# Performance work log

Measured on AMD Instinct MI355X. Metric: run time of the kernel, lower is better.

## Reference

```python
import jax, jax.numpy as jnp
import numpy as np

B, L, D, H = 2, 2048, 1024, 16
HD = D // H
HID = 4 * D
EPS = 1e-5


def setup_inputs() -> dict:
    key = jax.random.key(0)
    ks = jax.random.split(key, 16)
    s = 0.02
    inp = {
        "x": jax.random.normal(ks[0], (B, L, D), jnp.float32),
        "mask": jnp.triu(jnp.ones((L, L), bool), k=1),  # True above diagonal -> masked
        "wq": jax.random.normal(ks[1], (D, D), jnp.float32) * s,
        "wk": jax.random.normal(ks[2], (D, D), jnp.float32) * s,
        "wv": jax.random.normal(ks[3], (D, D), jnp.float32) * s,
        "wo": jax.random.normal(ks[4], (D, D), jnp.float32) * s,
        "ln1_g": jnp.ones((D,), jnp.float32),
        "ln1_b": jnp.zeros((D,), jnp.float32),
        "ln2_g": jnp.ones((D,), jnp.float32),
        "ln2_b": jnp.zeros((D,), jnp.float32),
        "w1": jax.random.normal(ks[5], (HID, D), jnp.float32) * s,
        "b1": jnp.zeros((HID,), jnp.float32),
        "wg": jax.random.normal(ks[6], (HID, D), jnp.float32) * s,
        "w2": jax.random.normal(ks[7], (D, HID), jnp.float32) * s,
        "b2": jnp.zeros((D,), jnp.float32),
    }
    return inp


def _layernorm(x, g, b):
    mu = jnp.mean(x, axis=-1, keepdims=True)
    var = jnp.mean(jnp.square(x - mu), axis=-1, keepdims=True)
    return (x - mu) * jax.lax.rsqrt(var + EPS) * g + b


def _attention(h, mask, wq, wk, wv, wo):
    b, l, d = h.shape
    scale = HD ** -0.5
    # torch Linear: y = x @ W.T (W is [out, in])
    q = (h @ wq.T).reshape(b, l, H, HD)
    k = (h @ wk.T).reshape(b, l, H, HD)
    v = (h @ wv.T).reshape(b, l, H, HD)
    attn = jnp.einsum("bqhd,bkhd->bhqk", q, k) * scale
    attn = jnp.where(mask[None, None, :, :], -jnp.inf, attn)
    pos_bias = jnp.arange(l, dtype=attn.dtype) * 0.01  # additive bias along key axis
    attn = attn + pos_bias[None, None, None, :]
    attn = jax.nn.softmax(attn, axis=-1)
    out = jnp.einsum("bhqk,bkhd->bqhd", attn, v).reshape(b, l, d)
    return out @ wo.T


def _ffn(h, w1, b1, wg, w2, b2):
    return (jax.nn.silu(h @ w1.T + b1) * (h @ wg.T)) @ w2.T + b2


def reference(x, mask, wq, wk, wv, wo, ln1_g, ln1_b, ln2_g, ln2_b, w1, b1, wg, w2, b2):
    x = x + _attention(_layernorm(x, ln1_g, ln1_b), mask, wq, wk, wv, wo)
    x = x + _ffn(_layernorm(x, ln2_g, ln2_b), w1, b1, wg, w2, b2)
    return x
```

## Files before the change

### kernel.cpp

```cpp
#include <hip/hip_runtime.h>

#define ML   2048
#define MD   1024
#define MH   16
#define MHD  64
#define MB   2
#define MM   4096
#define MHID 4096

typedef unsigned short u16;
typedef short bf16x8 __attribute__((ext_vector_type(8)));
typedef float f32x4 __attribute__((ext_vector_type(4)));

__device__ __forceinline__ u16 f2bf(float f) {
    union { float f; unsigned u; } c; c.f = f;
    unsigned r = c.u + 0x7fffu + ((c.u >> 16) & 1u);
    return (u16)(r >> 16);
}
__device__ __forceinline__ float bf2f(u16 h) {
    union { unsigned u; float f; } c; c.u = ((unsigned)h) << 16;
    return c.f;
}

__device__ __forceinline__ void async_copy16(const u16* g, u16* l) {
    __builtin_amdgcn_global_load_lds(
        (const __attribute__((address_space(1))) void*)g,
        (__attribute__((address_space(3))) void*)l, 16, 0, 0);
}

struct ConvPack {
    const float* src[13];
    u16* dst[13];
    int n[13];
    int start[14];
};

__global__ __launch_bounds__(256)
void conv_all(ConvPack p)
{
    const int bx = blockIdx.x;
    int seg = 0;
    while (seg < 12 && bx >= p.start[seg + 1]) ++seg;
    const int local = bx - p.start[seg];
    const int idx = (local * 256 + threadIdx.x) * 8;
    if (idx >= p.n[seg]) return;
    const float* in = p.src[seg];
    const float4 a = *(const float4*)(in + idx);
    const float4 b = *(const float4*)(in + idx + 4);
    union { bf16x8 v; u16 s[8]; } u;
    u.s[0] = f2bf(a.x); u.s[1] = f2bf(a.y); u.s[2] = f2bf(a.z); u.s[3] = f2bf(a.w);
    u.s[4] = f2bf(b.x); u.s[5] = f2bf(b.y); u.s[6] = f2bf(b.z); u.s[7] = f2bf(b.w);
    *(bf16x8*)&p.dst[seg][idx] = u.v;
}

template<int MI, int NI>
__device__ __forceinline__ void gemm_core(
    const u16* __restrict__ A, const u16* __restrict__ Bm,
    int m0, int n0, int lda, int ldb, int K,
    u16* As, u16* Bs, f32x4 (&acc)[MI][NI])
{
    constexpr int TM = MI * 32;
    constexpr int TN = NI * 32;
    const int tid  = threadIdx.x;
    const int wave = tid >> 6, lane = tid & 63;
    const int wm = wave & 1, wn = wave >> 1;
    const int l15 = lane & 15, quad = lane >> 4;

    const int srow = wave * 16 + (lane >> 2);
    const int scol = (lane & 3) * 8;
    const u16* Ag = A  + (size_t)(m0 + srow) * lda + scol;
    const u16* Bg = Bm + (size_t)(n0 + srow) * ldb + scol;
    u16* Asw = As + srow * 32 + scol;
    u16* Bsw = Bs + srow * 32 + scol;

    f32x4 zero4 = {0.f, 0.f, 0.f, 0.f};
#pragma unroll
    for (int mi = 0; mi < MI; ++mi)
#pragma unroll
        for (int ni = 0; ni < NI; ++ni) acc[mi][ni] = zero4;

    for (int k0 = 0; k0 < K; k0 += 32) {
        __syncthreads();
#pragma unroll
        for (int p = 0; p < TM / 64; ++p)
            async_copy16(Ag + k0 + (size_t)p * 64 * lda, Asw + p * 64 * 32);
#pragma unroll
        for (int p = 0; p < TN / 64; ++p)
            async_copy16(Bg + k0 + (size_t)p * 64 * ldb, Bsw + p * 64 * 32);
        __syncthreads();

        bf16x8 af[MI], bfr[NI];
#pragma unroll
        for (int mi = 0; mi < MI; ++mi)
            af[mi] = *(const bf16x8*)&As[(wm * MI * 16 + mi * 16 + l15) * 32 + quad * 8];
#pragma unroll
        for (int ni = 0; ni < NI; ++ni)
            bfr[ni] = *(const bf16x8*)&Bs[(wn * NI * 16 + ni * 16 + l15) * 32 + quad * 8];
#pragma unroll
        for (int mi = 0; mi < MI; ++mi)
#pragma unroll
            for (int ni = 0; ni < NI; ++ni)
                acc[mi][ni] = __builtin_amdgcn_mfma_f32_16x16x32_bf16(
                    af[mi], bfr[ni], acc[mi][ni], 0, 0, 0);
    }
}

__global__ __launch_bounds__(256)
void ln_kernel(const float* __restrict__ xin,
               const u16* __restrict__ g, const u16* __restrict__ bb,
               u16* __restrict__ out,
               const u16* __restrict__ rbias, float* __restrict__ oinit)
{
    const int row = blockIdx.x;
    const int tid = threadIdx.x;
    const float4 t = *(const float4*)(xin + (size_t)row * MD + tid * 4);
    float v[4] = {t.x, t.y, t.z, t.w};
    if (oinit) {
        const ushort4 rb = *(const ushort4*)&rbias[tid * 4];
        float4 oi;
        oi.x = v[0] + bf2f(rb.x);
        oi.y = v[1] + bf2f(rb.y);
        oi.z = v[2] + bf2f(rb.z);
        oi.w = v[3] + bf2f(rb.w);
        *(float4*)&oinit[(size_t)row * MD + tid * 4] = oi;
    }
    float s  = v[0] + v[1] + v[2] + v[3];
    float s2 = v[0]*v[0] + v[1]*v[1] + v[2]*v[2] + v[3]*v[3];
#pragma unroll
    for (int off = 1; off < 64; off <<= 1) {
        s  += __shfl_xor(s,  off);
        s2 += __shfl_xor(s2, off);
    }
    __shared__ float red[8];
    const int wave = tid >> 6, lane = tid & 63;
    if (lane == 0) { red[wave] = s; red[4 + wave] = s2; }
    __syncthreads();
    s  = red[0] + red[1] + red[2] + red[3];
    s2 = red[4] + red[5] + red[6] + red[7];
    const float mu  = s * (1.0f / MD);
    const float var = fmaxf(s2 * (1.0f / MD) - mu * mu, 0.0f);
    const float rs  = rsqrtf(var + 1e-5f);
    const ushort4 gv = *(const ushort4*)&g[tid * 4];
    const ushort4 bv = *(const ushort4*)&bb[tid * 4];
    ushort4 o;
    o.x = f2bf((v[0] - mu) * rs * bf2f(gv.x) + bf2f(bv.x));
    o.y = f2bf((v[1] - mu) * rs * bf2f(gv.y) + bf2f(bv.y));
    o.z = f2bf((v[2] - mu) * rs * bf2f(gv.z) + bf2f(bv.z));
    o.w = f2bf((v[3] - mu) * rs * bf2f(gv.w) + bf2f(bv.w));
    *(ushort4*)&out[(size_t)row * MD + tid * 4] = o;
}

__global__ __launch_bounds__(256, 2)
void gemm_qkv(const u16* __restrict__ ln, const u16* __restrict__ wq,
              const u16* __restrict__ wk, const u16* __restrict__ wv,
              u16* __restrict__ q, u16* __restrict__ k, u16* __restrict__ vt)
{
    __shared__ __align__(16) u16 As[128 * 32];
    __shared__ __align__(16) u16 Bs[128 * 32];
    const int z = blockIdx.z;
    const u16* Bm = (z == 0) ? wq : (z == 1) ? wk : wv;
    const int m0 = blockIdx.x * 128, n0 = blockIdx.y * 128;
    f32x4 acc[4][4];
    gemm_core<4, 4>(ln, Bm, m0, n0, MD, MD, MD, As, Bs, acc);

    const int tid = threadIdx.x;
    const int wave = tid >> 6, lane = tid & 63;
    const int wm = wave & 1, wn = wave >> 1, l15 = lane & 15, quad = lane >> 4;
    if (z < 2) {
        u16* out = (z == 0) ? q : k;
        const float scale = (z == 0) ? 0.125f : 1.0f;
#pragma unroll
        for (int mi = 0; mi < 4; ++mi)
#pragma unroll
            for (int ni = 0; ni < 4; ++ni)
#pragma unroll
                for (int r = 0; r < 4; ++r) {
                    const int row = m0 + wm * 64 + mi * 16 + quad * 4 + r;
                    const int col = n0 + wn * 64 + ni * 16 + l15;
                    out[(size_t)row * MD + col] = f2bf(acc[mi][ni][r] * scale);
                }
    } else {
#pragma unroll
        for (int mi = 0; mi < 4; ++mi)
#pragma unroll
            for (int ni = 0; ni < 4; ++ni) {
                const int row0 = m0 + wm * 64 + mi * 16 + quad * 4;
                const int col  = n0 + wn * 64 + ni * 16 + l15;
                const int bb = row0 >> 11, l = row0 & (ML - 1);
                const int hh = col >> 6,  hd = col & (MHD - 1);
                ushort4 pk;
                pk.x = f2bf(acc[mi][ni][0]);
                pk.y = f2bf(acc[mi][ni][1]);
                pk.z = f2bf(acc[mi][ni][2]);
                pk.w = f2bf(acc[mi][ni][3]);
                *(ushort4*)&vt[((size_t)(bb * MH + hh) * MHD + hd) * ML + l] = pk;
            }
    }
}

__global__ __launch_bounds__(256, 2)
void attn_kernel(const u16* __restrict__ Q, const u16* __restrict__ Kb,
                 const u16* __restrict__ Vt, u16* __restrict__ O)
{
    __shared__ __align__(16) u16 Ks[64 * 64];
    __shared__ __align__(16) u16 Vs[64 * 64];
    __shared__ __align__(16) u16 Pl[4][16 * 72];
    const int tid = threadIdx.x, wave = tid >> 6, lane = tid & 63;
    const int quad = lane >> 4, l15 = lane & 15;
    const int idx = blockIdx.x;
    const int qt = (ML / 64 - 1) - (idx >> 5);
    const int hb = idx & 31;
    const int h = hb & 15, b = hb >> 4;
    const int q0 = qt * 64;
    const int qrow = q0 + wave * 16;
    const float L2E = 1.44269504f;
    const float C1 = 0.01f * L2E;
    const float C2 = -32.0f * L2E;

    u16* Plw = Pl[wave];

    const size_t qoff = ((size_t)(b * ML + qrow + l15)) * MD + h * MHD + quad * 8;
    const bf16x8 aq0 = *(const bf16x8*)&Q[qoff];
    const bf16x8 aq1 = *(const bf16x8*)&Q[qoff + 32];

    const int str = tid >> 3;
    const int sj  = tid & 7;
    const int sjx = (sj ^ (str & 7)) * 8;
    const u16* Kg = Kb + (size_t)(b * ML) * MD + h * MHD;
    const u16* Vg = Vt + (size_t)((b * MH + h) * MHD) * ML;

    const int rsw0 = ((quad    ) ^ (l15 & 7)) * 8;
    const int rsw1 = ((quad + 4) ^ (l15 & 7)) * 8;

    bf16x8 onesf;
    {
        const short v = (l15 == 0) ? (short)0x3F80 : (short)0;
        onesf = (bf16x8){v, v, v, v, v, v, v, v};
    }

    f32x4 zero4 = {0.f, 0.f, 0.f, 0.f};
    f32x4 Oacc[4];
    f32x4 lsum = zero4;
#pragma unroll
    for (int i = 0; i < 4; ++i) Oacc[i] = zero4;

    for (int kt = 0; kt <= qt; ++kt) {
        const int k0 = kt * 64;

        __syncthreads();
        async_copy16(Kg + (size_t)(k0 + str) * MD + sjx,        Ks + tid * 8);
        async_copy16(Kg + (size_t)(k0 + 32 + str) * MD + sjx,   Ks + 2048 + tid * 8);
        async_copy16(Vg + (size_t)str * ML + k0 + sjx,          Vs + tid * 8);
        async_copy16(Vg + (size_t)(32 + str) * ML + k0 + sjx,   Vs + 2048 + tid * 8);
        __syncthreads();

        f32x4 s[4];
#pragma unroll
        for (int jn = 0; jn < 4; ++jn) {
            const int krow = (jn * 16 + l15) * 64;
            const bf16x8 k0f = *(const bf16x8*)&Ks[krow + rsw0];
            const bf16x8 k1f = *(const bf16x8*)&Ks[krow + rsw1];
            f32x4 z = zero4;
            z = __builtin_amdgcn_mfma_f32_16x16x32_bf16(aq0, k0f, z, 0, 0, 0);
            z = __builtin_amdgcn_mfma_f32_16x16x32_bf16(aq1, k1f, z, 0, 0, 0);
            s[jn] = z;
        }

        const bool diag = (kt == qt);
#pragma unroll
        for (int jn = 0; jn < 4; ++jn) {
            const int key = k0 + jn * 16 + l15;
            const float pbm = fmaf((float)key, C1, C2);
#pragma unroll
            for (int r = 0; r < 4; ++r) {
                float val = fmaf(s[jn][r], L2E, pbm);
                if (diag && key > qrow + quad * 4 + r) val = -30000.f;
                union { float f; unsigned u; } c;
                c.f = exp2f(val);
                Plw[(quad * 4 + r) * 72 + jn * 16 + l15] = (u16)(c.u >> 16);
            }
        }

        bf16x8 vv[4][2];
#pragma unroll
        for (int j = 0; j < 4; ++j) {
            const int vrow = (j * 16 + l15) * 64;
            vv[j][0] = *(const bf16x8*)&Vs[vrow + rsw0];
            vv[j][1] = *(const bf16x8*)&Vs[vrow + rsw1];
        }

        const bf16x8 ap0 = *(const bf16x8*)&Plw[l15 * 72 + quad * 8];
        const bf16x8 ap1 = *(const bf16x8*)&Plw[l15 * 72 + 32 + quad * 8];
#pragma unroll
        for (int j = 0; j < 4; ++j) {
            Oacc[j] = __builtin_amdgcn_mfma_f32_16x16x32_bf16(ap0, vv[j][0], Oacc[j], 0, 0, 0);
            Oacc[j] = __builtin_amdgcn_mfma_f32_16x16x32_bf16(ap1, vv[j][1], Oacc[j], 0, 0, 0);
        }
        lsum = __builtin_amdgcn_mfma_f32_16x16x32_bf16(ap0, onesf, lsum, 0, 0, 0);
        lsum = __builtin_amdgcn_mfma_f32_16x16x32_bf16(ap1, onesf, lsum, 0, 0, 0);
    }

#pragma unroll
    for (int r = 0; r < 4; ++r) {
        const float l = __shfl(lsum[r], lane & 48);
        const float inv = 1.0f / l;
        const int row = qrow + quad * 4 + r;
#pragma unroll
        for (int j = 0; j < 4; ++j) {
            const int col = h * MHD + j * 16 + l15;
            O[((size_t)(b * ML + row)) * MD + col] = f2bf(Oacc[j][r] * inv);
        }
    }
}

__global__ __launch_bounds__(256, 2)
void gemm_wo(const u16* __restrict__ ao, const u16* __restrict__ wo,
             const float* __restrict__ x, float* __restrict__ h1)
{
    __shared__ __align__(16) u16 As[64 * 32];
    __shared__ __align__(16) u16 Bs[128 * 32];
    const int m0 = blockIdx.x * 64, n0 = blockIdx.y * 128;
    f32x4 acc[2][4];
    gemm_core<2, 4>(ao, wo, m0, n0, MD, MD, MD, As, Bs, acc);
    const int tid = threadIdx.x;
    const int wave = tid >> 6, lane = tid & 63;
    const int wm = wave & 1, wn = wave >> 1, l15 = lane & 15, quad = lane >> 4;
#pragma unroll
    for (int mi = 0; mi < 2; ++mi)
#pragma unroll
        for (int ni = 0; ni < 4; ++ni)
#pragma unroll
            for (int r = 0; r < 4; ++r) {
                const int row = m0 + wm * 32 + mi * 16 + quad * 4 + r;
                const int col = n0 + wn * 64 + ni * 16 + l15;
                const size_t idx = (size_t)row * MD + col;
                h1[idx] = acc[mi][ni][r] + x[idx];
            }
}

__global__ __launch_bounds__(256, 2)
void gemm_ug(const u16* __restrict__ ln, const u16* __restrict__ w1,
             const u16* __restrict__ wg, const u16* __restrict__ b1,
             u16* __restrict__ hf)
{
    __shared__ __align__(16) u16 As[128 * 32];
    __shared__ __align__(16) u16 B1s[128 * 32];
    __shared__ __align__(16) u16 B2s[128 * 32];
    const int m0 = blockIdx.x * 128, n0 = blockIdx.y * 128;
    const int tid = threadIdx.x;
    const int wave = tid >> 6, lane = tid & 63;
    const int wm = wave & 1, wn = wave >> 1;
    const int l15 = lane & 15, quad = lane >> 4;

    const int srow = wave * 16 + (lane >> 2);
    const int scol = (lane & 3) * 8;
    const u16* Ag  = ln + (size_t)(m0 + srow) * MD + scol;
    const u16* B1g = w1 + (size_t)(n0 + srow) * MD + scol;
    const u16* B2g = wg + (size_t)(n0 + srow) * MD + scol;
    u16* Asw  = As  + srow * 32 + scol;
    u16* B1sw = B1s + srow * 32 + scol;
    u16* B2sw = B2s + srow * 32 + scol;

    f32x4 zero4 = {0.f, 0.f, 0.f, 0.f};
    f32x4 au[4][4], ag[4][4];
#pragma unroll
    for (int mi = 0; mi < 4; ++mi)
#pragma unroll
        for (int ni = 0; ni < 4; ++ni) { au[mi][ni] = zero4; ag[mi][ni] = zero4; }

    for (int k0 = 0; k0 < MD; k0 += 32) {
        __syncthreads();
#pragma unroll
        for (int p = 0; p < 2; ++p) {
            async_copy16(Ag  + k0 + (size_t)p * 64 * MD, Asw  + p * 64 * 32);
            async_copy16(B1g + k0 + (size_t)p * 64 * MD, B1sw + p * 64 * 32);
            async_copy16(B2g + k0 + (size_t)p * 64 * MD, B2sw + p * 64 * 32);
        }
        __syncthreads();

        bf16x8 af[4], f1[4], f2[4];
#pragma unroll
        for (int mi = 0; mi < 4; ++mi)
            af[mi] = *(const bf16x8*)&As[(wm * 64 + mi * 16 + l15) * 32 + quad * 8];
#pragma unroll
        for (int ni = 0; ni < 4; ++ni) {
            f1[ni] = *(const bf16x8*)&B1s[(wn * 64 + ni * 16 + l15) * 32 + quad * 8];
            f2[ni] = *(const bf16x8*)&B2s[(wn * 64 + ni * 16 + l15) * 32 + quad * 8];
        }
#pragma unroll
        for (int mi = 0; mi < 4; ++mi)
#pragma unroll
            for (int ni = 0; ni < 4; ++ni) {
                au[mi][ni] = __builtin_amdgcn_mfma_f32_16x16x32_bf16(
                    af[mi], f1[ni], au[mi][ni], 0, 0, 0);
                ag[mi][ni] = __builtin_amdgcn_mfma_f32_16x16x32_bf16(
                    af[mi], f2[ni], ag[mi][ni], 0, 0, 0);
            }
    }

#pragma unroll
    for (int mi = 0; mi < 4; ++mi)
#pragma unroll
        for (int ni = 0; ni < 4; ++ni)
#pragma unroll
            for (int r = 0; r < 4; ++r) {
                const int row = m0 + wm * 64 + mi * 16 + quad * 4 + r;
                const int col = n0 + wn * 64 + ni * 16 + l15;
                const float uv = au[mi][ni][r] + bf2f(b1[col]);
                const float si = uv / (1.0f + __expf(-uv));
                hf[(size_t)row * MHID + col] = f2bf(si * ag[mi][ni][r]);
            }
}

__global__ __launch_bounds__(256, 2)
void gemm_w2(const u16* __restrict__ hf, const u16* __restrict__ w2,
             float* __restrict__ out)
{
    __shared__ __align__(16) u16 As[128 * 32];
    __shared__ __align__(16) u16 Bs[128 * 32];
    const int m0 = blockIdx.x * 128, n0 = blockIdx.y * 128;
    const int kz = blockIdx.z * 2048;
    f32x4 acc[4][4];
    gemm_core<4, 4>(hf + kz, w2 + kz, m0, n0, MHID, MHID, 2048, As, Bs, acc);
    const int tid = threadIdx.x;
    const int wave = tid >> 6, lane = tid & 63;
    const int wm = wave & 1, wn = wave >> 1, l15 = lane & 15, quad = lane >> 4;
#pragma unroll
    for (int mi = 0; mi < 4; ++mi)
#pragma unroll
        for (int ni = 0; ni < 4; ++ni)
#pragma unroll
            for (int r = 0; r < 4; ++r) {
                const int row = m0 + wm * 64 + mi * 16 + quad * 4 + r;
                const int col = n0 + wn * 64 + ni * 16 + l15;
                unsafeAtomicAdd(&out[(size_t)row * MD + col], acc[mi][ni][r]);
            }
}

extern "C" void kernel_launch(void* const* d_in, const int* in_sizes, int n_in,
                              void* d_out, int out_size, void* d_ws, size_t ws_size,
                              hipStream_t stream)
{
    const float* x    = (const float*)d_in[0];
    const float* wq   = (const float*)d_in[2];
    const float* wk   = (const float*)d_in[3];
    const float* wv   = (const float*)d_in[4];
    const float* wo   = (const float*)d_in[5];
    const float* ln1g = (const float*)d_in[6];
    const float* ln1b = (const float*)d_in[7];
    const float* ln2g = (const float*)d_in[8];
    const float* ln2b = (const float*)d_in[9];
    const float* w1   = (const float*)d_in[10];
    const float* b1   = (const float*)d_in[11];
    const float* wgp  = (const float*)d_in[12];
    const float* w2   = (const float*)d_in[13];
    const float* b2   = (const float*)d_in[14];
    float* out = (float*)d_out;

    char* ws = (char*)d_ws;
    u16*  wqb  = (u16*)(ws);
    u16*  wkb  = (u16*)(ws + ((size_t)2  << 20));
    u16*  wvb  = (u16*)(ws + ((size_t)4  << 20));
    u16*  wob  = (u16*)(ws + ((size_t)6  << 20));
    u16*  w1b  = (u16*)(ws + ((size_t)8  << 20));
    u16*  wgb  = (u16*)(ws + ((size_t)16 << 20));
    u16*  w2b  = (u16*)(ws + ((size_t)24 << 20));
    char* vec  = ws + ((size_t)32 << 20);
    u16*  l1g  = (u16*)(vec);
    u16*  l1b  = (u16*)(vec + 4096);
    u16*  l2g  = (u16*)(vec + 8192);
    u16*  l2b  = (u16*)(vec + 12288);
    u16*  b1b  = (u16*)(vec + 16384);
    u16*  b2b  = (u16*)(vec + 24576);
    u16*   ln  = (u16*)(ws + ((size_t)33 << 20));
    u16*   q   = (u16*)(ws + ((size_t)41 << 20));
    u16*   k   = (u16*)(ws + ((size_t)49 << 20));
    u16*   vt  = (u16*)(ws + ((size_t)57 << 20));
    u16*   ao  = ln;
    float* h1  = (float*)(ws + ((size_t)41 << 20));
    u16*   hf  = (u16*)(ws + ((size_t)89 << 20));

    const int NW = MD * MD;
    const int NF = MHID * MD;
    ConvPack cp;
    const float* srcs[13] = {wq, wk, wv, wo, w1, wgp, w2, ln1g, ln1b, ln2g, ln2b, b1, b2};
    u16* dsts[13]         = {wqb, wkb, wvb, wob, w1b, wgb, w2b, l1g, l1b, l2g, l2b, b1b, b2b};
    int  ns[13]           = {NW, NW, NW, NW, NF, NF, NF, MD, MD, MD, MD, MHID, MD};
    int start = 0;
    for (int i = 0; i < 13; ++i) {
        cp.src[i] = srcs[i]; cp.dst[i] = dsts[i]; cp.n[i] = ns[i];
        cp.start[i] = start;
        start += (ns[i] + 2047) / 2048;
    }
    cp.start[13] = start;
    conv_all<<<start, 256, 0, stream>>>(cp);

    ln_kernel<<<MM, 256, 0, stream>>>(x, l1g, l1b, ln, nullptr, nullptr);
    gemm_qkv<<<dim3(MM / 128, MD / 128, 3), 256, 0, stream>>>(ln, wqb, wkb, wvb, q, k, vt);
    attn_kernel<<<(ML / 64) * MH * MB, 256, 0, stream>>>(q, k, vt, ao);
    gemm_wo<<<dim3(MM / 64, MD / 128), 256, 0, stream>>>(ao, wob, x, h1);
    ln_kernel<<<MM, 256, 0, stream>>>(h1, l2g, l2b, ln, b2b, out);
    gemm_ug<<<dim3(MM / 128, MHID / 128), 256, 0, stream>>>(ln, w1b, wgb, b1b, hf);
    gemm_w2<<<dim3(MM / 128, MD / 128, 2), 256, 0, stream>>>(hf, w2b, out);
}
```

Measured before the change: 398.0 us.

## Rewrite up/gate GEMM with 256-row tiles, double-buffered swizzled LDS and LDS epilogue exchange

The fused up/gate projection kernel now uses 512 threads and 256x128 output tiles with K=64 steps. It double-buffers the LDS stages so the next tile's async loads overlap the current MFMAs, and XOR-swizzles the LDS layout to avoid bank conflicts. Instead of each wave computing both the up and gate tiles, half the waves compute up and half compute gate, then swap partial results through LDS in the epilogue to apply SiLU. The aim is more data reuse per load, fewer syncs and hidden load latency, at the cost of 128KB of LDS (which caps occupancy) and an extra LDS round trip.

```diff
diff --git a/kernel.cpp b/kernel.cpp
--- a/kernel.cpp
+++ b/kernel.cpp
@@ -338,78 +338,136 @@
             }
 }
 
-__global__ __launch_bounds__(256, 2)
-void gemm_ug(const u16* __restrict__ ln, const u16* __restrict__ w1,
-             const u16* __restrict__ wg, const u16* __restrict__ b1,
-             u16* __restrict__ hf)
-{
-    __shared__ __align__(16) u16 As[128 * 32];
-    __shared__ __align__(16) u16 B1s[128 * 32];
-    __shared__ __align__(16) u16 B2s[128 * 32];
-    const int m0 = blockIdx.x * 128, n0 = blockIdx.y * 128;
+__global__ __launch_bounds__(512, 2)
+void gemm_ug256(const u16* __restrict__ ln, const u16* __restrict__ w1,
+                const u16* __restrict__ wg, const u16* __restrict__ b1,
+                u16* __restrict__ hf)
+{
+    __shared__ __align__(16) u16 smem[4][16384];
     const int tid = threadIdx.x;
     const int wave = tid >> 6, lane = tid & 63;
-    const int wm = wave & 1, wn = wave >> 1;
+    const int wm = wave >> 2, wn = wave & 3;
     const int l15 = lane & 15, quad = lane >> 4;
-
-    const int srow = wave * 16 + (lane >> 2);
-    const int scol = (lane & 3) * 8;
-    const u16* Ag  = ln + (size_t)(m0 + srow) * MD + scol;
-    const u16* B1g = w1 + (size_t)(n0 + srow) * MD + scol;
-    const u16* B2g = wg + (size_t)(n0 + srow) * MD + scol;
-    u16* Asw  = As  + srow * 32 + scol;
-    u16* B1sw = B1s + srow * 32 + scol;
-    u16* B2sw = B2s + srow * 32 + scol;
+    const int m0 = blockIdx.x * 256, n0 = blockIdx.y * 128;
+
+    const int str = tid >> 3;
+    const int sjx = ((tid & 7) ^ (str & 7)) * 8;
+    const u16* Ag  = ln + (size_t)(m0 + str) * MD + sjx;
+    const u16* B1g = w1 + (size_t)(n0 + str) * MD + sjx;
+    const u16* B2g = wg + (size_t)(n0 + str) * MD + sjx;
 
     f32x4 zero4 = {0.f, 0.f, 0.f, 0.f};
-    f32x4 au[4][4], ag[4][4];
-#pragma unroll
-    for (int mi = 0; mi < 4; ++mi)
-#pragma unroll
-        for (int ni = 0; ni < 4; ++ni) { au[mi][ni] = zero4; ag[mi][ni] = zero4; }
-
-    for (int k0 = 0; k0 < MD; k0 += 32) {
+    f32x4 acc[8][4];
+#pragma unroll
+    for (int mi = 0; mi < 8; ++mi)
+#pragma unroll
+        for (int ni = 0; ni < 4; ++ni) acc[mi][ni] = zero4;
+
+#define UG_STAGE(d, k0)                                                        \
+    do {                                                                       \
+        _Pragma("unroll")                                                      \
+        for (int p = 0; p < 4; ++p)                                            \
+            async_copy16(Ag + (size_t)p * 64 * MD + (k0),                      \
+                         &smem[d][p * 4096 + tid * 8]);                        \
+        _Pragma("unroll")                                                      \
+        for (int p = 0; p < 2; ++p)                                            \
+            async_copy16(B1g + (size_t)p * 64 * MD + (k0),                     \
+                         &smem[2 + (d)][p * 4096 + tid * 8]);                  \
+        _Pragma("unroll")                                                      \
+        for (int p = 0; p < 2; ++p)                                            \
+            async_copy16(B2g + (size_t)p * 64 * MD + (k0),                     \
+                         &smem[2 + (d)][(p + 2) * 4096 + tid * 8]);            \
+    } while (0)
+
+    UG_STAGE(0, 0);
+    __syncthreads();
+
+    for (int t = 0; t < 16; ++t) {
+        const int d = t & 1;
+        const u16* Abuf = smem[d];
+        const u16* Bbuf = smem[2 + d];
+
+        bf16x8 bfr[4][2], af0[4][2];
+#pragma unroll
+        for (int ni = 0; ni < 4; ++ni)
+#pragma unroll
+            for (int kh = 0; kh < 2; ++kh)
+                bfr[ni][kh] = *(const bf16x8*)&Bbuf[(wn * 64 + ni * 16 + l15) * 64
+                                                    + ((kh * 4 + quad) ^ (l15 & 7)) * 8];
+#pragma unroll
+        for (int mi = 0; mi < 4; ++mi)
+#pragma unroll
+            for (int kh = 0; kh < 2; ++kh)
+                af0[mi][kh] = *(const bf16x8*)&Abuf[(wm * 128 + mi * 16 + l15) * 64
+                                                    + ((kh * 4 + quad) ^ (l15 & 7)) * 8];
+
+        if (t < 15) UG_STAGE(d ^ 1, (t + 1) * 64);
+
+        __builtin_amdgcn_s_setprio(1);
+#pragma unroll
+        for (int mi = 0; mi < 4; ++mi)
+#pragma unroll
+            for (int ni = 0; ni < 4; ++ni) {
+                acc[mi][ni] = __builtin_amdgcn_mfma_f32_16x16x32_bf16(
+                    af0[mi][0], bfr[ni][0], acc[mi][ni], 0, 0, 0);
+                acc[mi][ni] = __builtin_amdgcn_mfma_f32_16x16x32_bf16(
+                    af0[mi][1], bfr[ni][1], acc[mi][ni], 0, 0, 0);
+            }
+        __builtin_amdgcn_s_setprio(0);
+        __builtin_amdgcn_s_barrier();
+
+        bf16x8 af1[4][2];
+#pragma unroll
+        for (int mi = 0; mi < 4; ++mi)
+#pragma unroll
+            for (int kh = 0; kh < 2; ++kh)
+                af1[mi][kh] = *(const bf16x8*)&Abuf[(wm * 128 + (mi + 4) * 16 + l15) * 64
+                                                    + ((kh * 4 + quad) ^ (l15 & 7)) * 8];
+        __builtin_amdgcn_s_setprio(1);
+#pragma unroll
+        for (int mi = 0; mi < 4; ++mi)
+#pragma unroll
+            for (int ni = 0; ni < 4; ++ni) {
+                acc[mi + 4][ni] = __builtin_amdgcn_mfma_f32_16x16x32_bf16(
+                    af1[mi][0], bfr[ni][0], acc[mi + 4][ni], 0, 0, 0);
+                acc[mi + 4][ni] = __builtin_amdgcn_mfma_f32_16x16x32_bf16(
+                    af1[mi][1], bfr[ni][1], acc[mi + 4][ni], 0, 0, 0);
+            }
+        __builtin_amdgcn_s_setprio(0);
+
         __syncthreads();
-#pragma unroll
-        for (int p = 0; p < 2; ++p) {
-            async_copy16(Ag  + k0 + (size_t)p * 64 * MD, Asw  + p * 64 * 32);
-            async_copy16(B1g + k0 + (size_t)p * 64 * MD, B1sw + p * 64 * 32);
-            async_copy16(B2g + k0 + (size_t)p * 64 * MD, B2sw + p * 64 * 32);
-        }
-        __syncthreads();
-
-        bf16x8 af[4], f1[4], f2[4];
-#pragma unroll
-        for (int mi = 0; mi < 4; ++mi)
-            af[mi] = *(const bf16x8*)&As[(wm * 64 + mi * 16 + l15) * 32 + quad * 8];
-#pragma unroll
-        for (int ni = 0; ni < 4; ++ni) {
-            f1[ni] = *(const bf16x8*)&B1s[(wn * 64 + ni * 16 + l15) * 32 + quad * 8];
-            f2[ni] = *(const bf16x8*)&B2s[(wn * 64 + ni * 16 + l15) * 32 + quad * 8];
-        }
-#pragma unroll
-        for (int mi = 0; mi < 4; ++mi)
+    }
+#undef UG_STAGE
+
+    float* X = (float*)&smem[0][0];
+    if (wn < 2) {
+        float* Xw = X + (wm * 2 + wn) * 8192;
+#pragma unroll
+        for (int mi = 0; mi < 8; ++mi)
+#pragma unroll
+            for (int ni = 0; ni < 4; ++ni)
+#pragma unroll
+                for (int r = 0; r < 4; ++r)
+                    Xw[((mi * 4 + ni) * 4 + r) * 64 + lane] = acc[mi][ni][r];
+    }
+    __syncthreads();
+    if (wn >= 2) {
+        const float* Xw = X + (wm * 2 + (wn - 2)) * 8192;
+#pragma unroll
+        for (int mi = 0; mi < 8; ++mi)
 #pragma unroll
             for (int ni = 0; ni < 4; ++ni) {
-                au[mi][ni] = __builtin_amdgcn_mfma_f32_16x16x32_bf16(
-                    af[mi], f1[ni], au[mi][ni], 0, 0, 0);
-                ag[mi][ni] = __builtin_amdgcn_mfma_f32_16x16x32_bf16(
-                    af[mi], f2[ni], ag[mi][ni], 0, 0, 0);
-            }
-    }
-
-#pragma unroll
-    for (int mi = 0; mi < 4; ++mi)
-#pragma unroll
-        for (int ni = 0; ni < 4; ++ni)
-#pragma unroll
-            for (int r = 0; r < 4; ++r) {
-                const int row = m0 + wm * 64 + mi * 16 + quad * 4 + r;
-                const int col = n0 + wn * 64 + ni * 16 + l15;
-                const float uv = au[mi][ni][r] + bf2f(b1[col]);
-                const float si = uv / (1.0f + __expf(-uv));
-                hf[(size_t)row * MHID + col] = f2bf(si * ag[mi][ni][r]);
-            }
+                const int col = n0 + (wn - 2) * 64 + ni * 16 + l15;
+                const float bb1 = bf2f(b1[col]);
+#pragma unroll
+                for (int r = 0; r < 4; ++r) {
+                    const int row = m0 + wm * 128 + mi * 16 + quad * 4 + r;
+                    const float uv = Xw[((mi * 4 + ni) * 4 + r) * 64 + lane] + bb1;
+                    const float si = uv / (1.0f + __expf(-uv));
+                    hf[(size_t)row * MHID + col] = f2bf(si * acc[mi][ni][r]);
+                }
+            }
+    }
 }
 
 __global__ __launch_bounds__(256, 2)
@@ -500,6 +558,6 @@
     attn_kernel<<<(ML / 64) * MH * MB, 256, 0, stream>>>(q, k, vt, ao);
     gemm_wo<<<dim3(MM / 64, MD / 128), 256, 0, stream>>>(ao, wob, x, h1);
     ln_kernel<<<MM, 256, 0, stream>>>(h1, l2g, l2b, ln, b2b, out);
-    gemm_ug<<<dim3(MM / 128, MHID / 128), 256, 0, stream>>>(ln, w1b, wgb, b1b, hf);
+    gemm_ug256<<<dim3(MM / 256, MHID / 128), 512, 0, stream>>>(ln, w1b, wgb, b1b, hf);
     gemm_w2<<<dim3(MM / 128, MD / 128, 2), 256, 0, stream>>>(hf, w2b, out);
 }
```

Measured after the change: 408.3 us. +2.6%, slower.
